# Optimization experiments

Measured on AMD Instinct MI355X. Metric: run time of the kernel, lower is better.

Reference implementation:

```python
import jax, jax.numpy as jnp
import numpy as np

P, R, S = 512, 128, 128   # num_proposal, ref_length, src_length
K = 3                      # top-k per row/column
THRESHOLD = 0.05
MUTUAL = False
CONDITIONAL = True


def setup_inputs() -> dict:
    key = jax.random.key(0)
    k1, k2, k3, k4 = jax.random.split(key, 4)
    return {
        "matching_score_map": jax.random.normal(k1, (P, R, S), dtype=jnp.float32),
        "ref_knn_masks": jax.random.bernoulli(k2, 0.9, (P, R)),
        "src_knn_masks": jax.random.bernoulli(k3, 0.9, (P, S)),
        "node_corr_scores": jax.random.uniform(k4, (P,), dtype=jnp.float32),
    }


def reference(matching_score_map, ref_knn_masks, src_knn_masks, node_corr_scores):
    # matching_score_map: [P, R, S] log-scores -> exp, as in torch forward
    m = jnp.exp(matching_score_map)
    p, r, s = m.shape
    # corr_mask_map = ref_mask[:, :, None] & src_mask[:, None, :] -> [P, R, S]
    corr_mask_map = jnp.logical_and(ref_knn_masks[:, :, None], src_knn_masks[:, None, :])

    pidx = jnp.arange(p)[:, None, None]

    # top-k along src dim (dim=2), scatter back into a sparse score map
    ref_topk_scores, ref_topk_idx = jax.lax.top_k(m, K)           # [P, R, K]
    ridx = jnp.arange(r)[None, :, None]
    ref_score_map = jnp.zeros_like(m).at[pidx, ridx, ref_topk_idx].set(ref_topk_scores)

    # top-k along ref dim (dim=1): transpose, top_k, scatter, transpose back
    mt = jnp.swapaxes(m, 1, 2)                                    # [P, S, R]
    src_topk_scores, src_topk_idx = jax.lax.top_k(mt, K)          # [P, S, K]
    sidx = jnp.arange(s)[None, :, None]
    src_score_map = jnp.swapaxes(
        jnp.zeros_like(mt).at[pidx, sidx, src_topk_idx].set(src_topk_scores), 1, 2
    )

    ref_corr_map = jnp.logical_and(ref_score_map > THRESHOLD, corr_mask_map)
    src_corr_map = jnp.logical_and(src_score_map > THRESHOLD, corr_mask_map)

    score_map = (ref_score_map + src_score_map) * 0.5
    if MUTUAL:
        corr_map = jnp.logical_and(ref_corr_map, src_corr_map)
    else:
        corr_map = jnp.logical_or(ref_corr_map, src_corr_map)
    if CONDITIONAL:
        score_map = score_map * node_corr_scores[:, None, None]
    return score_map, corr_map
```

## Files before the change

kernel.cpp:

```cpp
#include <hip/hip_runtime.h>


typedef float  vf4 __attribute__((ext_vector_type(4)));
typedef int    vi4 __attribute__((ext_vector_type(4)));

constexpr int NP = 512;
constexpr int NR = 128;
constexpr int NS = 128;
constexpr int RS = NR * NS;
constexpr float THRESHOLD = 0.05f;
constexpr float NEG_INF = -3.4e38f;

__device__ __forceinline__ void top3_insert(float v, float& m0, float& m1, float& m2) {
    float n1 = __builtin_amdgcn_fmed3f(v, m0, m1);
    float n2 = __builtin_amdgcn_fmed3f(v, m1, m2);
    m0 = fmaxf(m0, v);
    m1 = n1; m2 = n2;
}

__device__ __forceinline__ void shfl_merge3(int d, float& m0, float& m1, float& m2) {
    float o0 = __shfl_xor(m0, d);
    float o1 = __shfl_xor(m1, d);
    float o2 = __shfl_xor(m2, d);
    top3_insert(o0, m0, m1, m2);
    top3_insert(o1, m0, m1, m2);
    top3_insert(o2, m0, m1, m2);
}

__global__ __launch_bounds__(512, 4) void fused_kernel(
    const float* __restrict__ in,
    const int*   __restrict__ rmask,
    const int*   __restrict__ smask,
    const float* __restrict__ ncs,
    float*       __restrict__ out)
{
    __shared__ vf4 tile4[RS / 4];
    const int p   = blockIdx.x;
    const int t   = threadIdx.x;
    const int row = t >> 2;
    const int q   = t & 3;

    const vf4* b4 = (const vf4*)(in + (size_t)p * RS);

    vf4 x[8];
    float r0 = NEG_INF, r1 = NEG_INF, r2 = NEG_INF;
    #pragma unroll
    for (int j = 0; j < 8; ++j) {
        int c4 = q + 4 * j;
        x[j] = __builtin_nontemporal_load(&b4[row * 32 + c4]);
        tile4[row * 32 + (c4 ^ (row & 31))] = x[j];
        top3_insert(x[j].x, r0, r1, r2);
        top3_insert(x[j].y, r0, r1, r2);
        top3_insert(x[j].z, r0, r1, r2);
        top3_insert(x[j].w, r0, r1, r2);
    }
    shfl_merge3(1, r0, r1, r2);
    shfl_merge3(2, r0, r1, r2);
    const float tr = r2;
    __syncthreads();

    float c2_third;
    {
        const int col = t >> 2, seg = t & 3;
        const int c4c = col >> 2, cw = col & 3;
        const float* tf = (const float*)tile4;
        float c0 = NEG_INF, c1 = NEG_INF, c2 = NEG_INF;
        #pragma unroll 8
        for (int i = 0; i < 32; ++i) {
            int r = 4 * seg + (i & 3) + 16 * (i >> 2);
            top3_insert(tf[r * 128 + ((c4c ^ (r & 31)) << 2) + cw], c0, c1, c2);
        }
        shfl_merge3(1, c0, c1, c2);
        shfl_merge3(2, c0, c1, c2);
        c2_third = c2;
    }
    __syncthreads();
    {
        float* thirds = (float*)tile4;
        if ((t & 3) == 0) thirds[t >> 2] = c2_third;
    }
    __syncthreads();

    const float* thirds = (const float*)tile4;
    const float halfnc = 0.5f * ncs[p];
    const float mrf    = (rmask[p * NR + row] != 0) ? 1.0f : 0.0f;
    vf4* sc4 = (vf4*)(out + (size_t)p * RS);
    vf4* co4 = (vf4*)(out + (size_t)(NP + p) * RS);
    const vi4* sm4 = (const vi4*)(smask + (size_t)p * NS);

    #pragma unroll
    for (int j = 0; j < 8; ++j) {
        int c4 = q + 4 * j;
        vf4 tc = ((const vf4*)thirds)[c4];
        vi4 ms = __builtin_nontemporal_load(&sm4[c4]);
        vf4 v  = x[j];
        vf4 sc, co;

        {   float e = __expf(v.x);
            float w = ((v.x >= tr) ? halfnc : 0.f) + ((v.x >= tc.x) ? halfnc : 0.f);
            sc.x = e * w;
            float mk = (ms.x != 0) ? mrf : 0.f;
            co.x = (e > THRESHOLD && w > 0.f) ? mk : 0.f; }
        {   float e = __expf(v.y);
            float w = ((v.y >= tr) ? halfnc : 0.f) + ((v.y >= tc.y) ? halfnc : 0.f);
            sc.y = e * w;
            float mk = (ms.y != 0) ? mrf : 0.f;
            co.y = (e > THRESHOLD && w > 0.f) ? mk : 0.f; }
        {   float e = __expf(v.z);
            float w = ((v.z >= tr) ? halfnc : 0.f) + ((v.z >= tc.z) ? halfnc : 0.f);
            sc.z = e * w;
            float mk = (ms.z != 0) ? mrf : 0.f;
            co.z = (e > THRESHOLD && w > 0.f) ? mk : 0.f; }
        {   float e = __expf(v.w);
            float w = ((v.w >= tr) ? halfnc : 0.f) + ((v.w >= tc.w) ? halfnc : 0.f);
            sc.w = e * w;
            float mk = (ms.w != 0) ? mrf : 0.f;
            co.w = (e > THRESHOLD && w > 0.f) ? mk : 0.f; }

        __builtin_nontemporal_store(sc, &sc4[row * 32 + c4]);
        __builtin_nontemporal_store(co, &co4[row * 32 + c4]);
    }
}

extern "C" void kernel_launch(void* const* d_in, const int* in_sizes, int n_in,
                              void* d_out, int out_size, void* d_ws, size_t ws_size,
                              hipStream_t stream) {
    const float* msm   = (const float*)d_in[0];
    const int*   rmask = (const int*)  d_in[1];
    const int*   smask = (const int*)  d_in[2];
    const float* ncs   = (const float*)d_in[3];
    float* out = (float*)d_out;

    fused_kernel<<<NP, 512, 0, stream>>>(msm, rmask, smask, ncs, out);
}
```

Before: 107.4 us.

## Compute column top-3 from global memory instead of staging tile in LDS

Drops the 64KB shared-memory tile and its swizzled writes. The column third-largest values are now computed directly from global loads, one strided scalar load per element, and stored into a small shared array. The row pass then reloads the same slice from global, relying on L2/cache hits. Nontemporal load and store hints are removed throughout. The aim is to lower LDS usage and raise occupancy, at the cost of reading the input twice and making uncoalesced column loads.

```diff
diff --git a/kernel.cpp b/kernel.cpp
--- a/kernel.cpp
+++ b/kernel.cpp
@@ -1,8 +1,8 @@
 #include <hip/hip_runtime.h>
 
 
-typedef float  vf4 __attribute__((ext_vector_type(4)));
-typedef int    vi4 __attribute__((ext_vector_type(4)));
+typedef float vf4 __attribute__((ext_vector_type(4)));
+typedef int   vi4 __attribute__((ext_vector_type(4)));
 
 constexpr int NP = 512;
 constexpr int NR = 128;
@@ -34,21 +34,31 @@
     const float* __restrict__ ncs,
     float*       __restrict__ out)
 {
-    __shared__ vf4 tile4[RS / 4];
-    const int p   = blockIdx.x;
-    const int t   = threadIdx.x;
-    const int row = t >> 2;
-    const int q   = t & 3;
+    __shared__ float thirds[NS];
+    const int p = blockIdx.x;
+    const int t = threadIdx.x;
+    const float* base = in + (size_t)p * RS;
 
-    const vf4* b4 = (const vf4*)(in + (size_t)p * RS);
+    {
+        const int col = t >> 2, seg = t & 3;
+        const float* cbase = base + col + seg * NS;
+        float c0 = NEG_INF, c1 = NEG_INF, c2 = NEG_INF;
+        #pragma unroll 8
+        for (int i = 0; i < 32; ++i)
+            top3_insert(cbase[i * 4 * NS], c0, c1, c2);
+        shfl_merge3(1, c0, c1, c2);
+        shfl_merge3(2, c0, c1, c2);
+        if (seg == 0) thirds[col] = c2;
+    }
+    __syncthreads();
 
+    const int row = t >> 2, q = t & 3;
+    const vf4* b4 = (const vf4*)base;
     vf4 x[8];
     float r0 = NEG_INF, r1 = NEG_INF, r2 = NEG_INF;
     #pragma unroll
     for (int j = 0; j < 8; ++j) {
-        int c4 = q + 4 * j;
-        x[j] = __builtin_nontemporal_load(&b4[row * 32 + c4]);
-        tile4[row * 32 + (c4 ^ (row & 31))] = x[j];
+        x[j] = b4[row * 32 + (q + 4 * j)];
         top3_insert(x[j].x, r0, r1, r2);
         top3_insert(x[j].y, r0, r1, r2);
         top3_insert(x[j].z, r0, r1, r2);
@@ -57,42 +67,19 @@
     shfl_merge3(1, r0, r1, r2);
     shfl_merge3(2, r0, r1, r2);
     const float tr = r2;
-    __syncthreads();
 
-    float c2_third;
-    {
-        const int col = t >> 2, seg = t & 3;
-        const int c4c = col >> 2, cw = col & 3;
-        const float* tf = (const float*)tile4;
-        float c0 = NEG_INF, c1 = NEG_INF, c2 = NEG_INF;
-        #pragma unroll 8
-        for (int i = 0; i < 32; ++i) {
-            int r = 4 * seg + (i & 3) + 16 * (i >> 2);
-            top3_insert(tf[r * 128 + ((c4c ^ (r & 31)) << 2) + cw], c0, c1, c2);
-        }
-        shfl_merge3(1, c0, c1, c2);
-        shfl_merge3(2, c0, c1, c2);
-        c2_third = c2;
-    }
-    __syncthreads();
-    {
-        float* thirds = (float*)tile4;
-        if ((t & 3) == 0) thirds[t >> 2] = c2_third;
-    }
-    __syncthreads();
-
-    const float* thirds = (const float*)tile4;
     const float halfnc = 0.5f * ncs[p];
     const float mrf    = (rmask[p * NR + row] != 0) ? 1.0f : 0.0f;
     vf4* sc4 = (vf4*)(out + (size_t)p * RS);
     vf4* co4 = (vf4*)(out + (size_t)(NP + p) * RS);
     const vi4* sm4 = (const vi4*)(smask + (size_t)p * NS);
+    const vf4* th4 = (const vf4*)thirds;
 
     #pragma unroll
     for (int j = 0; j < 8; ++j) {
         int c4 = q + 4 * j;
-        vf4 tc = ((const vf4*)thirds)[c4];
-        vi4 ms = __builtin_nontemporal_load(&sm4[c4]);
+        vf4 tc = th4[c4];
+        vi4 ms = sm4[c4];
         vf4 v  = x[j];
         vf4 sc, co;
 
@@ -117,8 +104,8 @@
             float mk = (ms.w != 0) ? mrf : 0.f;
             co.w = (e > THRESHOLD && w > 0.f) ? mk : 0.f; }
 
-        __builtin_nontemporal_store(sc, &sc4[row * 32 + c4]);
-        __builtin_nontemporal_store(co, &co4[row * 32 + c4]);
+        sc4[row * 32 + c4] = sc;
+        co4[row * 32 + c4] = co;
     }
 }
 
```

Result: faster. 102.2 us (-4.8%).
